# Kernel tuning notes

Measured on AMD Instinct MI355X. Metric: run time of the kernel, lower is better.

Reference implementation:

```python
import jax, jax.numpy as jnp
import numpy as np

# Instant-NGP hash-encoding constants
PI = np.array([1, 2654435761, 805459861], dtype=np.uint32)
NUM_LEVELS = 16
MIN_RES = 16
MAX_RES = 512
T = 524288  # max entries per level (2**19)
D_EMBED = 2
N_POINTS = 2097152

# 8 binary corner offsets of a unit cube, shape [8, 3]
CORNERS = np.array([[(c >> d) & 1 for d in range(3)] for c in range(8)], dtype=np.int32)


def level_params():
    """Static per-level resolution, table size, offset, hashed flag."""
    b = (MAX_RES / MIN_RES) ** (1.0 / (NUM_LEVELS - 1))
    res = [int(np.floor(MIN_RES * b ** i)) for i in range(NUM_LEVELS)]
    sizes = [min((r + 1) ** 3, T) for r in res]
    offsets = np.concatenate([[0], np.cumsum(sizes)[:-1]]).astype(np.int32)
    hashed = [(r + 1) ** 3 > T for r in res]
    return res, sizes, offsets, hashed


RES, SIZES, OFFSETS, HASHED = level_params()
TOTAL_ENTRIES = int(np.sum(SIZES))


def setup_inputs() -> dict:
    key = jax.random.key(0)
    k1, k2 = jax.random.split(key)
    coords = jax.random.uniform(k1, (N_POINTS, 3), dtype=jnp.float32)
    embeddings = jax.random.normal(k2, (TOTAL_ENTRIES, D_EMBED), dtype=jnp.float32)
    return {"coords": coords, "embeddings": embeddings}


def _encode(coords, embeddings):
    corners = jnp.asarray(CORNERS)            # [8, 3] int32
    corner_mask = jnp.asarray(CORNERS, bool)  # [8, 3]
    pi = jnp.asarray(PI)                      # [3] uint32
    outs = []
    for lvl in range(NUM_LEVELS):
        res = RES[lvl]
        scaled = coords * res                                   # [N, 3]
        base = jnp.floor(scaled)
        frac = scaled - base                                    # [N, 3]
        # integer corner coords, clipped to valid grid range [0, res]
        c = jnp.clip(base.astype(jnp.int32)[:, None, :] + corners[None], 0, res)  # [N, 8, 3]
        if HASHED[lvl]:
            h = c.astype(jnp.uint32) * pi                        # wraparound mul, [N, 8, 3]
            idx = (h[..., 0] ^ h[..., 1] ^ h[..., 2]) % jnp.uint32(SIZES[lvl])
            idx = idx.astype(jnp.int32)                          # [N, 8]
        else:
            s = res + 1
            idx = c[..., 0] + c[..., 1] * s + c[..., 2] * (s * s)  # [N, 8]
        emb = embeddings[OFFSETS[lvl] + idx]                     # gather: [N, 8, d_embed]
        # trilinear weights: prod over dims of frac (corner=1) or 1-frac (corner=0)
        w = jnp.prod(jnp.where(corner_mask[None], frac[:, None, :], 1.0 - frac[:, None, :]), axis=-1)  # [N, 8]
        outs.append(jnp.einsum("nc,ncd->nd", w, emb))            # [N, d_embed]
    return jnp.concatenate(outs, axis=-1)                        # [N, L*d_embed]


def reference(coords, embeddings):
    return _encode(coords, embeddings)
```

## Files before the change

kernel.cpp:

```cpp
#include <hip/hip_runtime.h>
#include <math.h>

namespace {
constexpr int NPTS = 1 << 21;
constexpr int NLVL = 16;
constexpr unsigned TMASK = 0x7FFFFu;
constexpr unsigned PI1 = 2654435761u;
constexpr unsigned PI2 = 805459861u;
constexpr int BLK = 512;
constexpr int PTS_PER_BLK = 1024;
constexpr int NBLK = NPTS / PTS_PER_BLK;
constexpr int NGRID = 7;
constexpr int NHASH = 9;
constexpr int BRES = 64;
constexpr int NBKT = BRES * BRES * BRES;

typedef float f2 __attribute__((ext_vector_type(2)));
typedef float f4 __attribute__((ext_vector_type(4)));
typedef unsigned u4 __attribute__((ext_vector_type(4)));

struct Params {
  float resf[NLVL];
  int off[NLVL];
  int cellOffB[NGRID];
  int hOffB[NHASH];
};

__device__ __forceinline__ int swz(int pt) { return (pt ^ (pt >> 3)) & 7; }

__device__ __forceinline__ unsigned bfrne(float x) {
  unsigned f = __float_as_uint(x);
  return (f + 0x7FFFu + ((f >> 16) & 1u)) >> 16;
}
__device__ __forceinline__ unsigned packbf(f2 e) {
  return bfrne(e.x) | (bfrne(e.y) << 16);
}
__device__ __forceinline__ float bflo(unsigned u) {
  return __uint_as_float(u << 16);
}
__device__ __forceinline__ float bfhi(unsigned u) {
  return __uint_as_float(u & 0xFFFF0000u);
}
__device__ __forceinline__ unsigned sel4(f4 v, int k) {
  float g = (k & 2) ? ((k & 1) ? v.w : v.z) : ((k & 1) ? v.y : v.x);
  return __float_as_uint(g);
}
__device__ __forceinline__ int bucket_of(float cx, float cy, float cz) {
  return (int)(cx * 64.f) + ((int)(cy * 64.f) << 6) + ((int)(cz * 64.f) << 12);
}
}

__global__ __launch_bounds__(256) void repack_grid(const f2* __restrict__ emb,
                                                   char* __restrict__ ws,
                                                   Params p) {
  int lvl = (int)blockIdx.y;
  float rf = p.resf[0];
  int off = p.off[0], cob = p.cellOffB[0];
  if (lvl == 1) { rf = p.resf[1]; off = p.off[1]; cob = p.cellOffB[1]; }
  if (lvl == 2) { rf = p.resf[2]; off = p.off[2]; cob = p.cellOffB[2]; }
  if (lvl == 3) { rf = p.resf[3]; off = p.off[3]; cob = p.cellOffB[3]; }
  if (lvl == 4) { rf = p.resf[4]; off = p.off[4]; cob = p.cellOffB[4]; }
  if (lvl == 5) { rf = p.resf[5]; off = p.off[5]; cob = p.cellOffB[5]; }
  if (lvl == 6) { rf = p.resf[6]; off = p.off[6]; cob = p.cellOffB[6]; }
  int res = (int)rf;
  int t = (int)blockIdx.x * 256 + (int)threadIdx.x;
  if (t >= res * res * res) return;
  int x = t % res, q = t / res, y = q % res, z = q / res;
  int s = res + 1, s2 = s * s;
  const f2* base = emb + off + (x + y * s + z * s2);
  u4 d0, d1;
  d0.x = packbf(base[0]);       d0.y = packbf(base[1]);
  d0.z = packbf(base[s]);       d0.w = packbf(base[s + 1]);
  d1.x = packbf(base[s2]);      d1.y = packbf(base[s2 + 1]);
  d1.z = packbf(base[s2 + s]);  d1.w = packbf(base[s2 + s + 1]);
  u4* dst = (u4*)(ws + (size_t)cob + (size_t)t * 32);
  dst[0] = d0; dst[1] = d1;
}

__global__ __launch_bounds__(256) void repack_hash(const f2* __restrict__ emb,
                                                   char* __restrict__ ws,
                                                   Params p) {
  int h = (int)blockIdx.y;
  int off = p.off[7], hob = p.hOffB[0];
  if (h == 1) { off = p.off[8]; hob = p.hOffB[1]; }
  if (h == 2) { off = p.off[9]; hob = p.hOffB[2]; }
  if (h == 3) { off = p.off[10]; hob = p.hOffB[3]; }
  if (h == 4) { off = p.off[11]; hob = p.hOffB[4]; }
  if (h == 5) { off = p.off[12]; hob = p.hOffB[5]; }
  if (h == 6) { off = p.off[13]; hob = p.hOffB[6]; }
  if (h == 7) { off = p.off[14]; hob = p.hOffB[7]; }
  if (h == 8) { off = p.off[15]; hob = p.hOffB[8]; }
  int t = (int)blockIdx.x * 256 + (int)threadIdx.x;
  ((unsigned*)(ws + (size_t)hob))[t] = packbf(emb[off + t]);
}

__global__ __launch_bounds__(256) void hist_k(const float* __restrict__ coords,
                                              unsigned* __restrict__ cnt) {
  int t = (int)blockIdx.x * 256 + (int)threadIdx.x;
  const f4* C = (const f4*)(coords + (size_t)t * 12);
  f4 a = C[0], b = C[1], c = C[2];
  atomicAdd(&cnt[bucket_of(a.x, a.y, a.z)], 1u);
  atomicAdd(&cnt[bucket_of(a.w, b.x, b.y)], 1u);
  atomicAdd(&cnt[bucket_of(b.z, b.w, c.x)], 1u);
  atomicAdd(&cnt[bucket_of(c.y, c.z, c.w)], 1u);
}

__global__ __launch_bounds__(256) void scan1_k(const unsigned* __restrict__ cnt,
                                               unsigned* __restrict__ scanA,
                                               unsigned* __restrict__ bsum) {
  __shared__ unsigned s[256];
  int t = (int)threadIdx.x, i = (int)blockIdx.x * 256 + t;
  unsigned v = cnt[i];
  s[t] = v;
  __syncthreads();
  for (int d = 1; d < 256; d <<= 1) {
    unsigned x = (t >= d) ? s[t - d] : 0u;
    __syncthreads();
    s[t] += x;
    __syncthreads();
  }
  scanA[i] = s[t] - v;
  if (t == 255) bsum[blockIdx.x] = s[255];
}

__global__ __launch_bounds__(1024) void scan2_k(unsigned* __restrict__ bsum) {
  __shared__ unsigned s[1024];
  int t = (int)threadIdx.x;
  unsigned v = bsum[t];
  s[t] = v;
  __syncthreads();
  for (int d = 1; d < 1024; d <<= 1) {
    unsigned x = (t >= d) ? s[t - d] : 0u;
    __syncthreads();
    s[t] += x;
    __syncthreads();
  }
  bsum[t] = s[t] - v;
}

__global__ __launch_bounds__(256) void scat_k(const float* __restrict__ coords,
                                              unsigned* __restrict__ scanA,
                                              const unsigned* __restrict__ bsum,
                                              f4* __restrict__ sorted) {
  int t = (int)blockIdx.x * 256 + (int)threadIdx.x;
  const f4* C = (const f4*)(coords + (size_t)t * 12);
  f4 a = C[0], b = C[1], c = C[2];
  unsigned n0 = (unsigned)(t * 4);
  int b0 = bucket_of(a.x, a.y, a.z);
  unsigned s0 = atomicAdd(&scanA[b0], 1u) + bsum[b0 >> 8];
  f4 v0; v0.x = a.x; v0.y = a.y; v0.z = a.z; v0.w = __uint_as_float(n0);
  sorted[s0] = v0;
  int b1 = bucket_of(a.w, b.x, b.y);
  unsigned s1 = atomicAdd(&scanA[b1], 1u) + bsum[b1 >> 8];
  f4 v1; v1.x = a.w; v1.y = b.x; v1.z = b.y; v1.w = __uint_as_float(n0 + 1u);
  sorted[s1] = v1;
  int b2 = bucket_of(b.z, b.w, c.x);
  unsigned s2 = atomicAdd(&scanA[b2], 1u) + bsum[b2 >> 8];
  f4 v2; v2.x = b.z; v2.y = b.w; v2.z = c.x; v2.w = __uint_as_float(n0 + 2u);
  sorted[s2] = v2;
  int b3 = bucket_of(c.y, c.z, c.w);
  unsigned s3 = atomicAdd(&scanA[b3], 1u) + bsum[b3 >> 8];
  f4 v3; v3.x = c.y; v3.y = c.z; v3.z = c.w; v3.w = __uint_as_float(n0 + 3u);
  sorted[s3] = v3;
}

struct GB {
  f4 l0, l1;
  float wx0, wx1, w00, w10, w01, w11;
};

template <int LVL>
__device__ __forceinline__ void gridb_issue(const Params& p,
                                            const char* __restrict__ ws,
                                            float cx, float cy, float cz,
                                            GB& s) {
  float rf = p.resf[LVL];
  int res = (int)rf;
  float sx = cx * rf, sy = cy * rf, sz = cz * rf;
  float bx = floorf(sx), by = floorf(sy), bz = floorf(sz);
  float fx = sx - bx, fy = sy - by, fz = sz - bz;
  int ix = (int)bx, iy = (int)by, iz = (int)bz;
  int cell = (iz * res + iy) * res + ix;
  const f4* src = (const f4*)(ws + (size_t)p.cellOffB[LVL] + (size_t)cell * 32);
  s.l0 = src[0]; s.l1 = src[1];
  float wy0 = 1.f - fy, wy1 = fy, wz0 = 1.f - fz, wz1 = fz;
  s.wx0 = 1.f - fx; s.wx1 = fx;
  s.w00 = wy0 * wz0; s.w10 = wy1 * wz0; s.w01 = wy0 * wz1; s.w11 = wy1 * wz1;
}

__device__ __forceinline__ f2 gridb_consume(const GB& s) {
  float a0 = 0.f, a1 = 0.f;
  unsigned u;
  u = __float_as_uint(s.l0.x); a0 = fmaf(s.wx0 * s.w00, bflo(u), a0); a1 = fmaf(s.wx0 * s.w00, bfhi(u), a1);
  u = __float_as_uint(s.l0.y); a0 = fmaf(s.wx1 * s.w00, bflo(u), a0); a1 = fmaf(s.wx1 * s.w00, bfhi(u), a1);
  u = __float_as_uint(s.l0.z); a0 = fmaf(s.wx0 * s.w10, bflo(u), a0); a1 = fmaf(s.wx0 * s.w10, bfhi(u), a1);
  u = __float_as_uint(s.l0.w); a0 = fmaf(s.wx1 * s.w10, bflo(u), a0); a1 = fmaf(s.wx1 * s.w10, bfhi(u), a1);
  u = __float_as_uint(s.l1.x); a0 = fmaf(s.wx0 * s.w01, bflo(u), a0); a1 = fmaf(s.wx0 * s.w01, bfhi(u), a1);
  u = __float_as_uint(s.l1.y); a0 = fmaf(s.wx1 * s.w01, bflo(u), a0); a1 = fmaf(s.wx1 * s.w01, bfhi(u), a1);
  u = __float_as_uint(s.l1.z); a0 = fmaf(s.wx0 * s.w11, bflo(u), a0); a1 = fmaf(s.wx0 * s.w11, bfhi(u), a1);
  u = __float_as_uint(s.l1.w); a0 = fmaf(s.wx1 * s.w11, bflo(u), a0); a1 = fmaf(s.wx1 * s.w11, bfhi(u), a1);
  f2 r; r.x = a0; r.y = a1;
  return r;
}

template <int LVL>
__device__ __forceinline__ f2 grid_direct(const Params& p,
                                          const f2* __restrict__ emb, float cx,
                                          float cy, float cz) {
  float rf = p.resf[LVL];
  int res = (int)rf;
  int s = res + 1, s2 = s * s;
  const f2* tab = emb + p.off[LVL];
  float sx = cx * rf, sy = cy * rf, sz = cz * rf;
  float bx = floorf(sx), by = floorf(sy), bz = floorf(sz);
  float fx = sx - bx, fy = sy - by, fz = sz - bz;
  int ix = (int)bx, iy = (int)by, iz = (int)bz;
  int bse = ix + iy * s + iz * s2;
  f2 e0 = tab[bse], e1 = tab[bse + 1];
  f2 e2 = tab[bse + s], e3 = tab[bse + s + 1];
  f2 e4 = tab[bse + s2], e5 = tab[bse + s2 + 1];
  f2 e6 = tab[bse + s2 + s], e7 = tab[bse + s2 + s + 1];
  float wx0 = 1.f - fx, wx1 = fx, wy0 = 1.f - fy, wy1 = fy;
  float wz0 = 1.f - fz, wz1 = fz;
  float w00 = wy0 * wz0, w10 = wy1 * wz0, w01 = wy0 * wz1, w11 = wy1 * wz1;
  float a0 = 0.f, a1 = 0.f;
  a0 = fmaf(wx0 * w00, e0.x, a0); a1 = fmaf(wx0 * w00, e0.y, a1);
  a0 = fmaf(wx1 * w00, e1.x, a0); a1 = fmaf(wx1 * w00, e1.y, a1);
  a0 = fmaf(wx0 * w10, e2.x, a0); a1 = fmaf(wx0 * w10, e2.y, a1);
  a0 = fmaf(wx1 * w10, e3.x, a0); a1 = fmaf(wx1 * w10, e3.y, a1);
  a0 = fmaf(wx0 * w01, e4.x, a0); a1 = fmaf(wx0 * w01, e4.y, a1);
  a0 = fmaf(wx1 * w01, e5.x, a0); a1 = fmaf(wx1 * w01, e5.y, a1);
  a0 = fmaf(wx0 * w11, e6.x, a0); a1 = fmaf(wx0 * w11, e6.y, a1);
  a0 = fmaf(wx1 * w11, e7.x, a0); a1 = fmaf(wx1 * w11, e7.y, a1);
  f2 r; r.x = a0; r.y = a1;
  return r;
}

struct HB {
  f4 cA0, cB0, cA1, cB1, cA2, cB2, cA3, cB3;
  float wA0, wB0, wA1, wB1, wA2, wB2, wA3, wB3;
  int kA0, kB0, kA1, kB1, kA2, kB2, kA3, kB3;
};

template <int LVL>
__device__ __forceinline__ void hashb_issue(const Params& p,
                                            const char* __restrict__ ws,
                                            float cx, float cy, float cz,
                                            HB& s) {
  float rf = p.resf[LVL];
  const f4* tab = (const f4*)(ws + (size_t)p.hOffB[LVL - 7]);
  float sx = cx * rf, sy = cy * rf, sz = cz * rf;
  float bx = floorf(sx), by = floorf(sy), bz = floorf(sz);
  float fx = sx - bx, fy = sy - by, fz = sz - bz;
  unsigned ix = (unsigned)(int)bx, iy = (unsigned)(int)by,
           iz = (unsigned)(int)bz;
  unsigned jx = ix + 1u;
  unsigned ty0 = iy * PI1, ty1 = ty0 + PI1;
  unsigned tz0 = iz * PI2, tz1 = tz0 + PI2;
  unsigned e00 = ty0 ^ tz0, e10 = ty1 ^ tz0, e01 = ty0 ^ tz1, e11 = ty1 ^ tz1;
  float wx0 = 1.f - fx, wx1 = fx, wy0 = 1.f - fy, wy1 = fy;
  float wz0 = 1.f - fz, wz1 = fz;
  float w00 = wy0 * wz0, w10 = wy1 * wz0, w01 = wy0 * wz1, w11 = wy1 * wz1;
  unsigned iA0 = (ix ^ e00) & TMASK, iB0 = (jx ^ e00) & TMASK;
  unsigned iA1 = (ix ^ e10) & TMASK, iB1 = (jx ^ e10) & TMASK;
  unsigned iA2 = (ix ^ e01) & TMASK, iB2 = (jx ^ e01) & TMASK;
  unsigned iA3 = (ix ^ e11) & TMASK, iB3 = (jx ^ e11) & TMASK;
  s.kA0 = (int)(iA0 & 3u); s.kB0 = (int)(iB0 & 3u);
  s.kA1 = (int)(iA1 & 3u); s.kB1 = (int)(iB1 & 3u);
  s.kA2 = (int)(iA2 & 3u); s.kB2 = (int)(iB2 & 3u);
  s.kA3 = (int)(iA3 & 3u); s.kB3 = (int)(iB3 & 3u);
  s.cA0 = tab[iA0 >> 2]; s.cA1 = tab[iA1 >> 2];
  s.cA2 = tab[iA2 >> 2]; s.cA3 = tab[iA3 >> 2];
  s.cB0 = s.cA0; s.cB1 = s.cA1; s.cB2 = s.cA2; s.cB3 = s.cA3;
  if ((ix & 3u) == 3u) {
    s.cB0 = tab[iB0 >> 2]; s.cB1 = tab[iB1 >> 2];
    s.cB2 = tab[iB2 >> 2]; s.cB3 = tab[iB3 >> 2];
  }
  s.wA0 = wx0 * w00; s.wB0 = wx1 * w00;
  s.wA1 = wx0 * w10; s.wB1 = wx1 * w10;
  s.wA2 = wx0 * w01; s.wB2 = wx1 * w01;
  s.wA3 = wx0 * w11; s.wB3 = wx1 * w11;
}

__device__ __forceinline__ void hbpair(f4 cA, f4 cB, int kA, int kB, float wA,
                                       float wB, float& a0, float& a1) {
  unsigned uA = sel4(cA, kA), uB = sel4(cB, kB);
  a0 = fmaf(wA, bflo(uA), a0); a1 = fmaf(wA, bfhi(uA), a1);
  a0 = fmaf(wB, bflo(uB), a0); a1 = fmaf(wB, bfhi(uB), a1);
}

__device__ __forceinline__ f2 hashb_consume(const HB& s) {
  float a0 = 0.f, a1 = 0.f;
  hbpair(s.cA0, s.cB0, s.kA0, s.kB0, s.wA0, s.wB0, a0, a1);
  hbpair(s.cA1, s.cB1, s.kA1, s.kB1, s.wA1, s.wB1, a0, a1);
  hbpair(s.cA2, s.cB2, s.kA2, s.kB2, s.wA2, s.wB2, a0, a1);
  hbpair(s.cA3, s.cB3, s.kA3, s.kB3, s.wA3, s.wB3, a0, a1);
  f2 r; r.x = a0; r.y = a1;
  return r;
}

struct HS {
  f4 lo0, hi0, lo1, hi1, lo2, hi2, lo3, hi3;
  float wA0, wB0, wA1, wB1, wA2, wB2, wA3, wB3;
  int oA0, oB0, oA1, oB1, oA2, oB2, oA3, oB3;
};

template <int LVL>
__device__ __forceinline__ void hash_issue(const Params& p,
                                           const f2* __restrict__ emb,
                                           float cx, float cy, float cz,
                                           HS& s) {
  float rf = p.resf[LVL];
  const f2* tab = emb + p.off[LVL];
  float sx = cx * rf, sy = cy * rf, sz = cz * rf;
  float bx = floorf(sx), by = floorf(sy), bz = floorf(sz);
  float fx = sx - bx, fy = sy - by, fz = sz - bz;
  unsigned ix = (unsigned)(int)bx, iy = (unsigned)(int)by,
           iz = (unsigned)(int)bz;
  unsigned jx = ix + 1u;
  unsigned ty0 = iy * PI1, ty1 = ty0 + PI1;
  unsigned tz0 = iz * PI2, tz1 = tz0 + PI2;
  unsigned e00 = ty0 ^ tz0, e10 = ty1 ^ tz0, e01 = ty0 ^ tz1, e11 = ty1 ^ tz1;
  float wx0 = 1.f - fx, wx1 = fx, wy0 = 1.f - fy, wy1 = fy;
  float wz0 = 1.f - fz, wz1 = fz;
  float w00 = wy0 * wz0, w10 = wy1 * wz0, w01 = wy0 * wz1, w11 = wy1 * wz1;
  unsigned iA, iB;
  iA = (ix ^ e00) & TMASK; iB = (jx ^ e00) & TMASK;
  s.oA0 = (int)(iA & 1u); s.oB0 = (int)(iB & 1u);
  s.lo0 = *(const f4*)(tab + (iA & ~1u)); s.hi0 = *(const f4*)(tab + (iB & ~1u));
  s.wA0 = wx0 * w00; s.wB0 = wx1 * w00;
  iA = (ix ^ e10) & TMASK; iB = (jx ^ e10) & TMASK;
  s.oA1 = (int)(iA & 1u); s.oB1 = (int)(iB & 1u);
  s.lo1 = *(const f4*)(tab + (iA & ~1u)); s.hi1 = *(const f4*)(tab + (iB & ~1u));
  s.wA1 = wx0 * w10; s.wB1 = wx1 * w10;
  iA = (ix ^ e01) & TMASK; iB = (jx ^ e01) & TMASK;
  s.oA2 = (int)(iA & 1u); s.oB2 = (int)(iB & 1u);
  s.lo2 = *(const f4*)(tab + (iA & ~1u)); s.hi2 = *(const f4*)(tab + (iB & ~1u));
  s.wA2 = wx0 * w01; s.wB2 = wx1 * w01;
  iA = (ix ^ e11) & TMASK; iB = (jx ^ e11) & TMASK;
  s.oA3 = (int)(iA & 1u); s.oB3 = (int)(iB & 1u);
  s.lo3 = *(const f4*)(tab + (iA & ~1u)); s.hi3 = *(const f4*)(tab + (iB & ~1u));
  s.wA3 = wx0 * w11; s.wB3 = wx1 * w11;
}

__device__ __forceinline__ void hpair2(f4 lo, f4 hi, int oA, int oB, float wA,
                                       float wB, float& a0, float& a1) {
  float eAx = oA ? lo.z : lo.x, eAy = oA ? lo.w : lo.y;
  float eBx = oB ? hi.z : hi.x, eBy = oB ? hi.w : hi.y;
  a0 = fmaf(wA, eAx, a0); a1 = fmaf(wA, eAy, a1);
  a0 = fmaf(wB, eBx, a0); a1 = fmaf(wB, eBy, a1);
}

__device__ __forceinline__ f2 hash_consume(const HS& s) {
  float a0 = 0.f, a1 = 0.f;
  hpair2(s.lo0, s.hi0, s.oA0, s.oB0, s.wA0, s.wB0, a0, a1);
  hpair2(s.lo1, s.hi1, s.oA1, s.oB1, s.wA1, s.wB1, a0, a1);
  hpair2(s.lo2, s.hi2, s.oA2, s.oB2, s.wA2, s.wB2, a0, a1);
  hpair2(s.lo3, s.hi3, s.oA3, s.oB3, s.wA3, s.wB3, a0, a1);
  f2 r; r.x = a0; r.y = a1;
  return r;
}

template <int LVL, int MODE>
__device__ __forceinline__ void do_phase(const Params& p,
                                         const f2* __restrict__ emb,
                                         const char* __restrict__ ws,
                                         const float* cx, const float* cy,
                                         const float* cz, int pt0, int pt1,
                                         unsigned* lds) {
  f2 r0, r1;
  if constexpr (LVL < NGRID) {
    if constexpr (MODE < 2) {
      GB s0, s1;
      gridb_issue<LVL>(p, ws, cx[0], cy[0], cz[0], s0);
      gridb_issue<LVL>(p, ws, cx[1], cy[1], cz[1], s1);
      r0 = gridb_consume(s0);
      r1 = gridb_consume(s1);
    } else {
      r0 = grid_direct<LVL>(p, emb, cx[0], cy[0], cz[0]);
      r1 = grid_direct<LVL>(p, emb, cx[1], cy[1], cz[1]);
    }
  } else {
    if constexpr (MODE == 0) {
      HB s0, s1;
      hashb_issue<LVL>(p, ws, cx[0], cy[0], cz[0], s0);
      hashb_issue<LVL>(p, ws, cx[1], cy[1], cz[1], s1);
      r0 = hashb_consume(s0);
      r1 = hashb_consume(s1);
    } else {
      HS s0, s1;
      hash_issue<LVL>(p, emb, cx[0], cy[0], cz[0], s0);
      hash_issue<LVL>(p, emb, cx[1], cy[1], cz[1], s1);
      r0 = hash_consume(s0);
      r1 = hash_consume(s1);
    }
  }
  lds[pt0 * 8 + ((LVL & 7) ^ swz(pt0))] = packbf(r0);
  lds[pt1 * 8 + ((LVL & 7) ^ swz(pt1))] = packbf(r1);
}

template <bool SORTED>
__device__ __forceinline__ void readout(float* __restrict__ out,
                                        const unsigned* lds,
                                        const unsigned* oiLds, int n0, int h,
                                        int tid) {
#pragma unroll
  for (int j = 0; j < 8; ++j) {
    int f = tid + BLK * j;
    int pt = f >> 2, k = f & 3;
    int s = swz(pt);
    unsigned u0 = lds[pt * 8 + ((2 * k) ^ s)];
    unsigned u1 = lds[pt * 8 + ((2 * k + 1) ^ s)];
    f4 o4; o4.x = bflo(u0); o4.y = bfhi(u0); o4.z = bflo(u1); o4.w = bfhi(u1);
    size_t base = SORTED ? (size_t)oiLds[pt] * 32 : (size_t)(n0 + pt) * 32;
    __builtin_nontemporal_store(o4, (f4*)(out + base + h * 16 + k * 4));
  }
}

template <int MODE, bool SORTED>
__global__ __launch_bounds__(BLK, 4) void henc(const float* __restrict__ coords,
                                               const f2* __restrict__ emb,
                                               float* __restrict__ out,
                                               const char* __restrict__ ws,
                                               const f4* __restrict__ sorted,
                                               Params p) {
  __shared__ unsigned lds[PTS_PER_BLK * 8];
  __shared__ unsigned oiLds[PTS_PER_BLK];
  const int tid = (int)threadIdx.x;
  const int n0 = (int)blockIdx.x * PTS_PER_BLK;
  const int pt0 = 2 * tid, pt1 = 2 * tid + 1;

  float cx[2], cy[2], cz[2];
  if constexpr (SORTED) {
    f4 s0 = sorted[n0 + pt0];
    f4 s1 = sorted[n0 + pt1];
    cx[0] = s0.x; cy[0] = s0.y; cz[0] = s0.z;
    cx[1] = s1.x; cy[1] = s1.y; cz[1] = s1.z;
    oiLds[pt0] = __float_as_uint(s0.w);
    oiLds[pt1] = __float_as_uint(s1.w);
  } else {
    const f2* C = (const f2*)(coords + (size_t)3 * (n0 + pt0));
    f2 q0 = __builtin_nontemporal_load(&C[0]);
    f2 q1 = __builtin_nontemporal_load(&C[1]);
    f2 q2 = __builtin_nontemporal_load(&C[2]);
    cx[0] = q0.x; cy[0] = q0.y; cz[0] = q1.x;
    cx[1] = q1.y; cy[1] = q2.x; cz[1] = q2.y;
  }

  do_phase<0, MODE>(p, emb, ws, cx, cy, cz, pt0, pt1, lds);
  do_phase<1, MODE>(p, emb, ws, cx, cy, cz, pt0, pt1, lds);
  do_phase<2, MODE>(p, emb, ws, cx, cy, cz, pt0, pt1, lds);
  do_phase<3, MODE>(p, emb, ws, cx, cy, cz, pt0, pt1, lds);
  do_phase<4, MODE>(p, emb, ws, cx, cy, cz, pt0, pt1, lds);
  do_phase<5, MODE>(p, emb, ws, cx, cy, cz, pt0, pt1, lds);
  do_phase<6, MODE>(p, emb, ws, cx, cy, cz, pt0, pt1, lds);
  do_phase<7, MODE>(p, emb, ws, cx, cy, cz, pt0, pt1, lds);
  __syncthreads();
  readout<SORTED>(out, lds, oiLds, n0, 0, tid);
  __syncthreads();

  do_phase<8, MODE>(p, emb, ws, cx, cy, cz, pt0, pt1, lds);
  do_phase<9, MODE>(p, emb, ws, cx, cy, cz, pt0, pt1, lds);
  do_phase<10, MODE>(p, emb, ws, cx, cy, cz, pt0, pt1, lds);
  do_phase<11, MODE>(p, emb, ws, cx, cy, cz, pt0, pt1, lds);
  do_phase<12, MODE>(p, emb, ws, cx, cy, cz, pt0, pt1, lds);
  do_phase<13, MODE>(p, emb, ws, cx, cy, cz, pt0, pt1, lds);
  do_phase<14, MODE>(p, emb, ws, cx, cy, cz, pt0, pt1, lds);
  do_phase<15, MODE>(p, emb, ws, cx, cy, cz, pt0, pt1, lds);
  __syncthreads();
  readout<SORTED>(out, lds, oiLds, n0, 1, tid);
}

extern "C" void kernel_launch(void* const* d_in, const int* in_sizes, int n_in,
                              void* d_out, int out_size, void* d_ws,
                              size_t ws_size, hipStream_t stream) {
  const float* coords = (const float*)d_in[0];
  const f2* emb = (const f2*)d_in[1];
  float* out = (float*)d_out;
  char* ws = (char*)d_ws;

  Params p;
  double b = pow(32.0, 1.0 / 15.0);
  long long cum = 0, cellCum = 0;
  int resMax = 64;
  for (int i = 0; i < NLVL; ++i) {
    int r = (int)floor(16.0 * pow(b, (double)i));
    p.resf[i] = (float)r;
    p.off[i] = (int)cum;
    long long e3 = (long long)(r + 1) * (r + 1) * (r + 1);
    cum += e3 > 524288 ? 524288 : e3;
    if (i < NGRID) {
      p.cellOffB[i] = (int)(cellCum * 32);
      cellCum += (long long)r * r * r;
      if (i == NGRID - 1) resMax = r;
    }
  }
  long long gridB = ((cellCum * 32 + 63) / 64) * 64;
  for (int h = 0; h < NHASH; ++h)
    p.hOffB[h] = (int)(gridB + (long long)h * (524288 * 4));
  size_t needB = (size_t)gridB;
  size_t needA = (size_t)(gridB + 9LL * 524288 * 4);

  size_t cntOff = (needA + 255) & ~(size_t)255;
  size_t scanOff = cntOff + (size_t)NBKT * 4;
  size_t bsumOff = scanOff + (size_t)NBKT * 4;
  size_t sortedOff = (bsumOff + 4096 + 255) & ~(size_t)255;
  size_t needS = sortedOff + (size_t)NPTS * 16;

  int mode = ws_size >= needA ? 0 : (ws_size >= needB ? 1 : 2);
  bool doSort = ws_size >= needS;

  if (mode < 2) {
    int bx = (resMax * resMax * resMax + 255) / 256;
    repack_grid<<<dim3(bx, NGRID), dim3(256), 0, stream>>>(emb, ws, p);
  }
  if (mode == 0) {
    repack_hash<<<dim3(524288 / 256, NHASH), dim3(256), 0, stream>>>(emb, ws,
                                                                     p);
    if (doSort) {
      unsigned* cnt = (unsigned*)(ws + cntOff);
      unsigned* scanA = (unsigned*)(ws + scanOff);
      unsigned* bsum = (unsigned*)(ws + bsumOff);
      f4* sorted = (f4*)(ws + sortedOff);
      hipMemsetAsync(cnt, 0, (size_t)NBKT * 4, stream);
      hist_k<<<dim3(NPTS / 4 / 256), dim3(256), 0, stream>>>(coords, cnt);
      scan1_k<<<dim3(NBKT / 256), dim3(256), 0, stream>>>(cnt, scanA, bsum);
      scan2_k<<<dim3(1), dim3(1024), 0, stream>>>(bsum);
      scat_k<<<dim3(NPTS / 4 / 256), dim3(256), 0, stream>>>(coords, scanA,
                                                             bsum, sorted);
      henc<0, true><<<dim3(NBLK), dim3(BLK), 0, stream>>>(coords, emb, out, ws,
                                                          sorted, p);
    } else {
      henc<0, false><<<dim3(NBLK), dim3(BLK), 0, stream>>>(coords, emb, out,
                                                           ws, nullptr, p);
    }
  } else if (mode == 1) {
    henc<1, false><<<dim3(NBLK), dim3(BLK), 0, stream>>>(coords, emb, out, ws,
                                                         nullptr, p);
  } else {
    henc<2, false><<<dim3(NBLK), dim3(BLK), 0, stream>>>(coords, emb, out, ws,
                                                         nullptr, p);
  }
}
```

Before: 520.5 us.

## Process one point per thread, merge repack kernels, load neighbor hash entry as scalar

The main encoding kernel now handles one point per thread instead of two, which halves points per block and doubles the block count, reducing per-thread register state and raising occupancy at the cost of less per-thread memory-level parallelism. The grid and hash repack kernels are fused into one launch covering all 16 levels to save a launch. In the hash path, the +x neighbor entry is fetched as a single 32-bit word only when it falls in a different 4-entry chunk, instead of a full 16-byte vector, which cuts register use and load width. Readout loops shrink to match the smaller block.

```diff
diff --git a/kernel.cpp b/kernel.cpp
--- a/kernel.cpp
+++ b/kernel.cpp
@@ -8,7 +8,7 @@
 constexpr unsigned PI1 = 2654435761u;
 constexpr unsigned PI2 = 805459861u;
 constexpr int BLK = 512;
-constexpr int PTS_PER_BLK = 1024;
+constexpr int PTS_PER_BLK = 512;
 constexpr int NBLK = NPTS / PTS_PER_BLK;
 constexpr int NGRID = 7;
 constexpr int NHASH = 9;
@@ -48,6 +48,47 @@
 __device__ __forceinline__ int bucket_of(float cx, float cy, float cz) {
   return (int)(cx * 64.f) + ((int)(cy * 64.f) << 6) + ((int)(cz * 64.f) << 12);
 }
+}
+
+__global__ __launch_bounds__(256) void repack_all(const f2* __restrict__ emb,
+                                                  char* __restrict__ ws,
+                                                  Params p) {
+  int y = (int)blockIdx.y;
+  int t = (int)blockIdx.x * 256 + (int)threadIdx.x;
+  if (y >= NGRID) {
+    int h = y - NGRID;
+    int off = p.off[7], hob = p.hOffB[0];
+    if (h == 1) { off = p.off[8]; hob = p.hOffB[1]; }
+    if (h == 2) { off = p.off[9]; hob = p.hOffB[2]; }
+    if (h == 3) { off = p.off[10]; hob = p.hOffB[3]; }
+    if (h == 4) { off = p.off[11]; hob = p.hOffB[4]; }
+    if (h == 5) { off = p.off[12]; hob = p.hOffB[5]; }
+    if (h == 6) { off = p.off[13]; hob = p.hOffB[6]; }
+    if (h == 7) { off = p.off[14]; hob = p.hOffB[7]; }
+    if (h == 8) { off = p.off[15]; hob = p.hOffB[8]; }
+    ((unsigned*)(ws + (size_t)hob))[t] = packbf(emb[off + t]);
+    return;
+  }
+  float rf = p.resf[0];
+  int off = p.off[0], cob = p.cellOffB[0];
+  if (y == 1) { rf = p.resf[1]; off = p.off[1]; cob = p.cellOffB[1]; }
+  if (y == 2) { rf = p.resf[2]; off = p.off[2]; cob = p.cellOffB[2]; }
+  if (y == 3) { rf = p.resf[3]; off = p.off[3]; cob = p.cellOffB[3]; }
+  if (y == 4) { rf = p.resf[4]; off = p.off[4]; cob = p.cellOffB[4]; }
+  if (y == 5) { rf = p.resf[5]; off = p.off[5]; cob = p.cellOffB[5]; }
+  if (y == 6) { rf = p.resf[6]; off = p.off[6]; cob = p.cellOffB[6]; }
+  int res = (int)rf;
+  if (t >= res * res * res) return;
+  int x = t % res, q = t / res, yy = q % res, z = q / res;
+  int s = res + 1, s2 = s * s;
+  const f2* base = emb + off + (x + yy * s + z * s2);
+  u4 d0, d1;
+  d0.x = packbf(base[0]);       d0.y = packbf(base[1]);
+  d0.z = packbf(base[s]);       d0.w = packbf(base[s + 1]);
+  d1.x = packbf(base[s2]);      d1.y = packbf(base[s2 + 1]);
+  d1.z = packbf(base[s2 + s]);  d1.w = packbf(base[s2 + s + 1]);
+  u4* dst = (u4*)(ws + (size_t)cob + (size_t)t * 32);
+  dst[0] = d0; dst[1] = d1;
 }
 
 __global__ __launch_bounds__(256) void repack_grid(const f2* __restrict__ emb,
@@ -75,23 +116,6 @@
   d1.z = packbf(base[s2 + s]);  d1.w = packbf(base[s2 + s + 1]);
   u4* dst = (u4*)(ws + (size_t)cob + (size_t)t * 32);
   dst[0] = d0; dst[1] = d1;
-}
-
-__global__ __launch_bounds__(256) void repack_hash(const f2* __restrict__ emb,
-                                                   char* __restrict__ ws,
-                                                   Params p) {
-  int h = (int)blockIdx.y;
-  int off = p.off[7], hob = p.hOffB[0];
-  if (h == 1) { off = p.off[8]; hob = p.hOffB[1]; }
-  if (h == 2) { off = p.off[9]; hob = p.hOffB[2]; }
-  if (h == 3) { off = p.off[10]; hob = p.hOffB[3]; }
-  if (h == 4) { off = p.off[11]; hob = p.hOffB[4]; }
-  if (h == 5) { off = p.off[12]; hob = p.hOffB[5]; }
-  if (h == 6) { off = p.off[13]; hob = p.hOffB[6]; }
-  if (h == 7) { off = p.off[14]; hob = p.hOffB[7]; }
-  if (h == 8) { off = p.off[15]; hob = p.hOffB[8]; }
-  int t = (int)blockIdx.x * 256 + (int)threadIdx.x;
-  ((unsigned*)(ws + (size_t)hob))[t] = packbf(emb[off + t]);
 }
 
 __global__ __launch_bounds__(256) void hist_k(const float* __restrict__ coords,
@@ -237,9 +261,11 @@
 }
 
 struct HB {
-  f4 cA0, cB0, cA1, cB1, cA2, cB2, cA3, cB3;
+  f4 cA0, cA1, cA2, cA3;
+  unsigned uB0, uB1, uB2, uB3;
   float wA0, wB0, wA1, wB1, wA2, wB2, wA3, wB3;
-  int kA0, kB0, kA1, kB1, kA2, kB2, kA3, kB3;
+  int kA0, kA1, kA2, kA3, kB0, kB1, kB2, kB3;
+  bool sameChunk;
 };
 
 template <int LVL>
@@ -249,6 +275,7 @@
                                             HB& s) {
   float rf = p.resf[LVL];
   const f4* tab = (const f4*)(ws + (size_t)p.hOffB[LVL - 7]);
+  const unsigned* t32 = (const unsigned*)tab;
   float sx = cx * rf, sy = cy * rf, sz = cz * rf;
   float bx = floorf(sx), by = floorf(sy), bz = floorf(sz);
   float fx = sx - bx, fy = sy - by, fz = sz - bz;
@@ -265,36 +292,39 @@
   unsigned iA1 = (ix ^ e10) & TMASK, iB1 = (jx ^ e10) & TMASK;
   unsigned iA2 = (ix ^ e01) & TMASK, iB2 = (jx ^ e01) & TMASK;
   unsigned iA3 = (ix ^ e11) & TMASK, iB3 = (jx ^ e11) & TMASK;
-  s.kA0 = (int)(iA0 & 3u); s.kB0 = (int)(iB0 & 3u);
-  s.kA1 = (int)(iA1 & 3u); s.kB1 = (int)(iB1 & 3u);
-  s.kA2 = (int)(iA2 & 3u); s.kB2 = (int)(iB2 & 3u);
-  s.kA3 = (int)(iA3 & 3u); s.kB3 = (int)(iB3 & 3u);
+  s.sameChunk = (ix & 3u) != 3u;
+  s.uB0 = 0u; s.uB1 = 0u; s.uB2 = 0u; s.uB3 = 0u;
+  if (!s.sameChunk) {
+    s.uB0 = t32[iB0]; s.uB1 = t32[iB1];
+    s.uB2 = t32[iB2]; s.uB3 = t32[iB3];
+  }
   s.cA0 = tab[iA0 >> 2]; s.cA1 = tab[iA1 >> 2];
   s.cA2 = tab[iA2 >> 2]; s.cA3 = tab[iA3 >> 2];
-  s.cB0 = s.cA0; s.cB1 = s.cA1; s.cB2 = s.cA2; s.cB3 = s.cA3;
-  if ((ix & 3u) == 3u) {
-    s.cB0 = tab[iB0 >> 2]; s.cB1 = tab[iB1 >> 2];
-    s.cB2 = tab[iB2 >> 2]; s.cB3 = tab[iB3 >> 2];
-  }
+  s.kA0 = (int)(iA0 & 3u); s.kA1 = (int)(iA1 & 3u);
+  s.kA2 = (int)(iA2 & 3u); s.kA3 = (int)(iA3 & 3u);
+  s.kB0 = (int)(iB0 & 3u); s.kB1 = (int)(iB1 & 3u);
+  s.kB2 = (int)(iB2 & 3u); s.kB3 = (int)(iB3 & 3u);
   s.wA0 = wx0 * w00; s.wB0 = wx1 * w00;
   s.wA1 = wx0 * w10; s.wB1 = wx1 * w10;
   s.wA2 = wx0 * w01; s.wB2 = wx1 * w01;
   s.wA3 = wx0 * w11; s.wB3 = wx1 * w11;
 }
 
-__device__ __forceinline__ void hbpair(f4 cA, f4 cB, int kA, int kB, float wA,
-                                       float wB, float& a0, float& a1) {
-  unsigned uA = sel4(cA, kA), uB = sel4(cB, kB);
+__device__ __forceinline__ void hbpair(f4 cA, unsigned uBl, int kA, int kB,
+                                       bool same, float wA, float wB,
+                                       float& a0, float& a1) {
+  unsigned uA = sel4(cA, kA);
+  unsigned uB = same ? sel4(cA, kB) : uBl;
   a0 = fmaf(wA, bflo(uA), a0); a1 = fmaf(wA, bfhi(uA), a1);
   a0 = fmaf(wB, bflo(uB), a0); a1 = fmaf(wB, bfhi(uB), a1);
 }
 
 __device__ __forceinline__ f2 hashb_consume(const HB& s) {
   float a0 = 0.f, a1 = 0.f;
-  hbpair(s.cA0, s.cB0, s.kA0, s.kB0, s.wA0, s.wB0, a0, a1);
-  hbpair(s.cA1, s.cB1, s.kA1, s.kB1, s.wA1, s.wB1, a0, a1);
-  hbpair(s.cA2, s.cB2, s.kA2, s.kB2, s.wA2, s.wB2, a0, a1);
-  hbpair(s.cA3, s.cB3, s.kA3, s.kB3, s.wA3, s.wB3, a0, a1);
+  hbpair(s.cA0, s.uB0, s.kA0, s.kB0, s.sameChunk, s.wA0, s.wB0, a0, a1);
+  hbpair(s.cA1, s.uB1, s.kA1, s.kB1, s.sameChunk, s.wA1, s.wB1, a0, a1);
+  hbpair(s.cA2, s.uB2, s.kA2, s.kB2, s.sameChunk, s.wA2, s.wB2, a0, a1);
+  hbpair(s.cA3, s.uB3, s.kA3, s.kB3, s.sameChunk, s.wA3, s.wB3, a0, a1);
   f2 r; r.x = a0; r.y = a1;
   return r;
 }
@@ -364,39 +394,30 @@
 template <int LVL, int MODE>
 __device__ __forceinline__ void do_phase(const Params& p,
                                          const f2* __restrict__ emb,
-                                         const char* __restrict__ ws,
-                                         const float* cx, const float* cy,
-                                         const float* cz, int pt0, int pt1,
+                                         const char* __restrict__ ws, float cx,
+                                         float cy, float cz, int pt,
                                          unsigned* lds) {
-  f2 r0, r1;
+  f2 r;
   if constexpr (LVL < NGRID) {
     if constexpr (MODE < 2) {
-      GB s0, s1;
-      gridb_issue<LVL>(p, ws, cx[0], cy[0], cz[0], s0);
-      gridb_issue<LVL>(p, ws, cx[1], cy[1], cz[1], s1);
-      r0 = gridb_consume(s0);
-      r1 = gridb_consume(s1);
+      GB s;
+      gridb_issue<LVL>(p, ws, cx, cy, cz, s);
+      r = gridb_consume(s);
     } else {
-      r0 = grid_direct<LVL>(p, emb, cx[0], cy[0], cz[0]);
-      r1 = grid_direct<LVL>(p, emb, cx[1], cy[1], cz[1]);
+      r = grid_direct<LVL>(p, emb, cx, cy, cz);
     }
   } else {
     if constexpr (MODE == 0) {
-      HB s0, s1;
-      hashb_issue<LVL>(p, ws, cx[0], cy[0], cz[0], s0);
-      hashb_issue<LVL>(p, ws, cx[1], cy[1], cz[1], s1);
-      r0 = hashb_consume(s0);
-      r1 = hashb_consume(s1);
+      HB s;
+      hashb_issue<LVL>(p, ws, cx, cy, cz, s);
+      r = hashb_consume(s);
     } else {
-      HS s0, s1;
-      hash_issue<LVL>(p, emb, cx[0], cy[0], cz[0], s0);
-      hash_issue<LVL>(p, emb, cx[1], cy[1], cz[1], s1);
-      r0 = hash_consume(s0);
-      r1 = hash_consume(s1);
+      HS s;
+      hash_issue<LVL>(p, emb, cx, cy, cz, s);
+      r = hash_consume(s);
     }
   }
-  lds[pt0 * 8 + ((LVL & 7) ^ swz(pt0))] = packbf(r0);
-  lds[pt1 * 8 + ((LVL & 7) ^ swz(pt1))] = packbf(r1);
+  lds[pt * 8 + ((LVL & 7) ^ swz(pt))] = packbf(r);
 }
 
 template <bool SORTED>
@@ -405,7 +426,7 @@
                                         const unsigned* oiLds, int n0, int h,
                                         int tid) {
 #pragma unroll
-  for (int j = 0; j < 8; ++j) {
+  for (int j = 0; j < 4; ++j) {
     int f = tid + BLK * j;
     int pt = f >> 2, k = f & 3;
     int s = swz(pt);
@@ -428,45 +449,39 @@
   __shared__ unsigned oiLds[PTS_PER_BLK];
   const int tid = (int)threadIdx.x;
   const int n0 = (int)blockIdx.x * PTS_PER_BLK;
-  const int pt0 = 2 * tid, pt1 = 2 * tid + 1;
-
-  float cx[2], cy[2], cz[2];
+  const int pt = tid;
+
+  float cx, cy, cz;
   if constexpr (SORTED) {
-    f4 s0 = sorted[n0 + pt0];
-    f4 s1 = sorted[n0 + pt1];
-    cx[0] = s0.x; cy[0] = s0.y; cz[0] = s0.z;
-    cx[1] = s1.x; cy[1] = s1.y; cz[1] = s1.z;
-    oiLds[pt0] = __float_as_uint(s0.w);
-    oiLds[pt1] = __float_as_uint(s1.w);
+    f4 s0 = sorted[n0 + pt];
+    cx = s0.x; cy = s0.y; cz = s0.z;
+    oiLds[pt] = __float_as_uint(s0.w);
   } else {
-    const f2* C = (const f2*)(coords + (size_t)3 * (n0 + pt0));
-    f2 q0 = __builtin_nontemporal_load(&C[0]);
-    f2 q1 = __builtin_nontemporal_load(&C[1]);
-    f2 q2 = __builtin_nontemporal_load(&C[2]);
-    cx[0] = q0.x; cy[0] = q0.y; cz[0] = q1.x;
-    cx[1] = q1.y; cy[1] = q2.x; cz[1] = q2.y;
-  }
-
-  do_phase<0, MODE>(p, emb, ws, cx, cy, cz, pt0, pt1, lds);
-  do_phase<1, MODE>(p, emb, ws, cx, cy, cz, pt0, pt1, lds);
-  do_phase<2, MODE>(p, emb, ws, cx, cy, cz, pt0, pt1, lds);
-  do_phase<3, MODE>(p, emb, ws, cx, cy, cz, pt0, pt1, lds);
-  do_phase<4, MODE>(p, emb, ws, cx, cy, cz, pt0, pt1, lds);
-  do_phase<5, MODE>(p, emb, ws, cx, cy, cz, pt0, pt1, lds);
-  do_phase<6, MODE>(p, emb, ws, cx, cy, cz, pt0, pt1, lds);
-  do_phase<7, MODE>(p, emb, ws, cx, cy, cz, pt0, pt1, lds);
+    cx = coords[3 * (n0 + pt) + 0];
+    cy = coords[3 * (n0 + pt) + 1];
+    cz = coords[3 * (n0 + pt) + 2];
+  }
+
+  do_phase<0, MODE>(p, emb, ws, cx, cy, cz, pt, lds);
+  do_phase<1, MODE>(p, emb, ws, cx, cy, cz, pt, lds);
+  do_phase<2, MODE>(p, emb, ws, cx, cy, cz, pt, lds);
+  do_phase<3, MODE>(p, emb, ws, cx, cy, cz, pt, lds);
+  do_phase<4, MODE>(p, emb, ws, cx, cy, cz, pt, lds);
+  do_phase<5, MODE>(p, emb, ws, cx, cy, cz, pt, lds);
+  do_phase<6, MODE>(p, emb, ws, cx, cy, cz, pt, lds);
+  do_phase<7, MODE>(p, emb, ws, cx, cy, cz, pt, lds);
   __syncthreads();
   readout<SORTED>(out, lds, oiLds, n0, 0, tid);
   __syncthreads();
 
-  do_phase<8, MODE>(p, emb, ws, cx, cy, cz, pt0, pt1, lds);
-  do_phase<9, MODE>(p, emb, ws, cx, cy, cz, pt0, pt1, lds);
-  do_phase<10, MODE>(p, emb, ws, cx, cy, cz, pt0, pt1, lds);
-  do_phase<11, MODE>(p, emb, ws, cx, cy, cz, pt0, pt1, lds);
-  do_phase<12, MODE>(p, emb, ws, cx, cy, cz, pt0, pt1, lds);
-  do_phase<13, MODE>(p, emb, ws, cx, cy, cz, pt0, pt1, lds);
-  do_phase<14, MODE>(p, emb, ws, cx, cy, cz, pt0, pt1, lds);
-  do_phase<15, MODE>(p, emb, ws, cx, cy, cz, pt0, pt1, lds);
+  do_phase<8, MODE>(p, emb, ws, cx, cy, cz, pt, lds);
+  do_phase<9, MODE>(p, emb, ws, cx, cy, cz, pt, lds);
+  do_phase<10, MODE>(p, emb, ws, cx, cy, cz, pt, lds);
+  do_phase<11, MODE>(p, emb, ws, cx, cy, cz, pt, lds);
+  do_phase<12, MODE>(p, emb, ws, cx, cy, cz, pt, lds);
+  do_phase<13, MODE>(p, emb, ws, cx, cy, cz, pt, lds);
+  do_phase<14, MODE>(p, emb, ws, cx, cy, cz, pt, lds);
+  do_phase<15, MODE>(p, emb, ws, cx, cy, cz, pt, lds);
   __syncthreads();
   readout<SORTED>(out, lds, oiLds, n0, 1, tid);
 }
@@ -510,13 +525,8 @@
   int mode = ws_size >= needA ? 0 : (ws_size >= needB ? 1 : 2);
   bool doSort = ws_size >= needS;
 
-  if (mode < 2) {
-    int bx = (resMax * resMax * resMax + 255) / 256;
-    repack_grid<<<dim3(bx, NGRID), dim3(256), 0, stream>>>(emb, ws, p);
-  }
   if (mode == 0) {
-    repack_hash<<<dim3(524288 / 256, NHASH), dim3(256), 0, stream>>>(emb, ws,
-                                                                     p);
+    repack_all<<<dim3(524288 / 256, NLVL), dim3(256), 0, stream>>>(emb, ws, p);
     if (doSort) {
       unsigned* cnt = (unsigned*)(ws + cntOff);
       unsigned* scanA = (unsigned*)(ws + scanOff);
@@ -535,6 +545,8 @@
                                                            ws, nullptr, p);
     }
   } else if (mode == 1) {
+    int bx = (resMax * resMax * resMax + 255) / 256;
+    repack_grid<<<dim3(bx, NGRID), dim3(256), 0, stream>>>(emb, ws, p);
     henc<1, false><<<dim3(NBLK), dim3(BLK), 0, stream>>>(coords, emb, out, ws,
                                                          nullptr, p);
   } else {
```

Result: faster. 467.7 us (-10.1%).
